# Optimization experiments

Measured on AMD Instinct MI355X. Metric: run time of the kernel, lower is better.

The kernel has to match this reference:

```python
import jax, jax.numpy as jnp
import numpy as np

N = 50000   # num_nodes
D = 128     # h_dim
R = 32      # num_rels * 2 (forward + inverse relations)
B = 8       # num_bases
E = 600000  # num_edges


def setup_inputs() -> dict:
    key = jax.random.key(0)
    ks = jax.random.split(key, 14)
    s = 1.0 / np.sqrt(D)
    return {
        "h_ids": jnp.arange(N, dtype=jnp.int32),
        "src": jax.random.randint(ks[0], (E,), 0, N),
        "dst": jax.random.randint(ks[1], (E,), 0, N),
        "etype": jax.random.randint(ks[2], (E,), 0, R),
        "norm": jax.random.uniform(ks[3], (E, 1), dtype=jnp.float32),
        "embedding": jax.random.normal(ks[4], (N, D), dtype=jnp.float32) * 0.05,
        "w_comp1": jax.random.normal(ks[5], (R, B), dtype=jnp.float32) * (1.0 / np.sqrt(B)),
        "bases1": jax.random.normal(ks[6], (B, D, D), dtype=jnp.float32) * s,
        "loop_w1": jax.random.normal(ks[7], (D, D), dtype=jnp.float32) * s,
        "bias1": jnp.zeros((D,), dtype=jnp.float32),
        "w_comp2": jax.random.normal(ks[8], (R, B), dtype=jnp.float32) * (1.0 / np.sqrt(B)),
        "bases2": jax.random.normal(ks[9], (B, D, D), dtype=jnp.float32) * s,
        "loop_w2": jax.random.normal(ks[10], (D, D), dtype=jnp.float32) * s,
        "bias2": jnp.zeros((D,), dtype=jnp.float32),
    }


def _rel_graph_conv(h, src, dst, etype, norm, w_comp, bases, loop_w, bias, act):
    # basis decomposition: W[r] = sum_b w_comp[r,b] * bases[b]
    W = jnp.einsum('rb,bio->rio', w_comp, bases)          # [R, D, D]
    # transform every node by every relation weight (dense GEMM)
    all_t = jnp.einsum('ni,rio->nro', h, W)               # [N, R, D]
    # per-edge gather of relation-specific transformed source features
    msg = all_t[src, etype] * norm                        # [E, D]
    # scatter-aggregate messages at destination nodes
    agg = jax.ops.segment_sum(msg, dst, num_segments=h.shape[0])  # [N, D]
    out = agg + h @ loop_w + bias                         # self-loop + bias
    return act(out) if act is not None else out


def reference(h_ids, src, dst, etype, norm, embedding,
              w_comp1, bases1, loop_w1, bias1,
              w_comp2, bases2, loop_w2, bias2):
    # EmbeddingLayer
    h = embedding[h_ids]                                  # [N, D]
    # hidden layer 0: relu activation (idx < num_hidden_layers-1)
    h = _rel_graph_conv(h, src, dst, etype, norm, w_comp1, bases1, loop_w1, bias1, jax.nn.relu)
    # hidden layer 1: no activation (last layer)
    h = _rel_graph_conv(h, src, dst, etype, norm, w_comp2, bases2, loop_w2, bias2, None)
    return h
```

## Files before the change

### kernel.cpp

```cpp
#include <hip/hip_runtime.h>

#define DD 128
#define NB 8
#define KTOT 1152

typedef unsigned int uint_t;
typedef __attribute__((ext_vector_type(8))) _Float16 half8v;
typedef __attribute__((ext_vector_type(2))) _Float16 half2v;
typedef __attribute__((ext_vector_type(4))) float f32x4;

static __device__ __forceinline__ void gld_lds16(const _Float16* g, _Float16* l)
{
  __builtin_amdgcn_global_load_lds(
      (const __attribute__((address_space(1))) void*)g,
      (__attribute__((address_space(3))) void*)l, 16, 0, 0);
}

static __device__ __forceinline__ half2v bc_h2(uint_t u)
{
  union { uint_t u; half2v h; } c; c.u = u; return c.h;
}

static __device__ __forceinline__ float fdot2(uint_t a, uint_t b, float acc)
{
#if __has_builtin(__builtin_amdgcn_fdot2)
  return __builtin_amdgcn_fdot2(bc_h2(a), bc_h2(b), acc, false);
#else
  half2v x = bc_h2(a), y = bc_h2(b);
  return acc + (float)x[0] * (float)y[0] + (float)x[1] * (float)y[1];
#endif
}

__global__ __launch_bounds__(256) void k_prep_w(
    const float* __restrict__ bases1, const float* __restrict__ loopw1,
    const float* __restrict__ bases2, const float* __restrict__ loopw2,
    _Float16* __restrict__ WcA)
{
  int i = blockIdx.x * 256 + threadIdx.x;
  if (i >= 2 * 36 * DD * 32) return;
  int layer = i / (36 * DD * 32);
  int rem   = i % (36 * DD * 32);
  int ks    = rem / (DD * 32);
  int rem2  = rem % (DD * 32);
  int feat  = rem2 / 32;
  int j     = rem2 % 32;
  int k     = ks * 32 + j;
  const float* basesL = layer ? bases2 : bases1;
  const float* loopwL = layer ? loopw2 : loopw1;
  float v;
  if (k < 1024) {
    int kk = k >> 3, b = k & 7;
    v = basesL[((size_t)b * DD + kk) * DD + feat];
  } else {
    v = loopwL[(size_t)(k - 1024) * DD + feat];
  }
  WcA[i] = (_Float16)v;
}

__global__ __launch_bounds__(256) void k_cast(
    const float* __restrict__ h, const int* __restrict__ ids,
    _Float16* __restrict__ hf, int N)
{
  int i = blockIdx.x * 256 + threadIdx.x;
  if (i >= N * (DD / 8)) return;
  int n  = i / (DD / 8);
  int k8 = (i % (DD / 8)) * 8;
  int row = ids ? ids[n] : n;
  const float* hp = h + (size_t)row * DD + k8;
  float4 v0 = *(const float4*)hp;
  float4 v1 = *(const float4*)(hp + 4);
  union { _Float16 e[8]; uint4 q; } p;
  p.e[0]=(_Float16)v0.x; p.e[1]=(_Float16)v0.y; p.e[2]=(_Float16)v0.z; p.e[3]=(_Float16)v0.w;
  p.e[4]=(_Float16)v1.x; p.e[5]=(_Float16)v1.y; p.e[6]=(_Float16)v1.z; p.e[7]=(_Float16)v1.w;
  *(uint4*)&hf[(size_t)n * DD + k8] = p.q;
}

__global__ __launch_bounds__(256) void k_zero(int* __restrict__ p, int n)
{
  int i = blockIdx.x * 256 + threadIdx.x;
  if (i < n) p[i] = 0;
}

__global__ __launch_bounds__(256) void k_hist(
    const int* __restrict__ dst, int* __restrict__ cnt, int E)
{
  int e = blockIdx.x * 256 + threadIdx.x;
  if (e < E) atomicAdd(&cnt[dst[e]], 1);
}

__global__ __launch_bounds__(256) void k_bsum(
    const int* __restrict__ cnt, int* __restrict__ bsum, int N)
{
  __shared__ int s[256];
  int i = blockIdx.x * 256 + threadIdx.x;
  s[threadIdx.x] = (i < N) ? ((cnt[i] + 1) & ~1) : 0;
  __syncthreads();
  for (int off = 128; off > 0; off >>= 1) {
    if (threadIdx.x < off) s[threadIdx.x] += s[threadIdx.x + off];
    __syncthreads();
  }
  if (threadIdx.x == 0) bsum[blockIdx.x] = s[0];
}

__global__ __launch_bounds__(256) void k_scanb(
    const int* __restrict__ bsum, int* __restrict__ boff, int nb)
{
  __shared__ int s[256];
  int t = threadIdx.x;
  int own = (t < nb) ? bsum[t] : 0;
  s[t] = own;
  __syncthreads();
  for (int off = 1; off < 256; off <<= 1) {
    int v = (t >= off) ? s[t - off] : 0;
    __syncthreads();
    s[t] += v;
    __syncthreads();
  }
  if (t < nb) boff[t] = s[t] - own;
}

__global__ __launch_bounds__(256) void k_scan3(
    const int* __restrict__ cnt, const int* __restrict__ boff,
    int* __restrict__ row_start, int N)
{
  __shared__ int s[256];
  int t = threadIdx.x;
  int i = blockIdx.x * 256 + t;
  int v = (i < N) ? ((cnt[i] + 1) & ~1) : 0;
  s[t] = v;
  __syncthreads();
  for (int off = 1; off < 256; off <<= 1) {
    int u = (t >= off) ? s[t - off] : 0;
    __syncthreads();
    s[t] += u;
    __syncthreads();
  }
  if (i < N) row_start[i] = boff[blockIdx.x] + s[t] - v;
}

__global__ __launch_bounds__(256) void k_pad(
    const int* __restrict__ rowst, const int* __restrict__ cnt,
    int* __restrict__ psrc, int N)
{
  int v = blockIdx.x * 256 + threadIdx.x;
  if (v < N && (cnt[v] & 1)) {
    int slot = rowst[v] + cnt[v];
    psrc[slot] = 0;
  }
}

__global__ __launch_bounds__(256) void k_place(
    const int* __restrict__ dst, const int* __restrict__ src,
    const int* __restrict__ etype, const float* __restrict__ norm,
    const int* __restrict__ row_start, int* __restrict__ cursor,
    int* __restrict__ psrc, int2* __restrict__ en, int E)
{
  int e = blockIdx.x * 256 + threadIdx.x;
  if (e < E) {
    int v = dst[e];
    int slot = row_start[v] + atomicAdd(&cursor[v], 1);
    psrc[slot] = src[e];
    en[slot] = make_int2(etype[e], __float_as_int(norm[e]));
  }
}

__global__ __launch_bounds__(256) void k_payload_pair(
    const int2* __restrict__ en,
    const float* __restrict__ wcomp1, const float* __restrict__ wcomp2,
    _Float16* __restrict__ c1, _Float16* __restrict__ c2, int npair)
{
  int i = blockIdx.x * 256 + threadIdx.x;
  if (i >= npair) return;
  int2 e0 = en[2 * i], e1 = en[2 * i + 1];
  float n0 = __int_as_float(e0.y), n1 = __int_as_float(e1.y);
  const float* w10 = wcomp1 + e0.x * NB;
  const float* w11 = wcomp1 + e1.x * NB;
  const float* w20 = wcomp2 + e0.x * NB;
  const float* w21 = wcomp2 + e1.x * NB;

  union { _Float16 h[16]; uint4 q[2]; } p;
  #pragma unroll
  for (int b = 0; b < NB; b++) {
    p.h[b * 2]     = (_Float16)(w10[b] * n0);
    p.h[b * 2 + 1] = (_Float16)(w11[b] * n1);
  }
  *(uint4*)&c1[(size_t)i * 16]     = p.q[0];
  *(uint4*)&c1[(size_t)i * 16 + 8] = p.q[1];
  #pragma unroll
  for (int b = 0; b < NB; b++) {
    p.h[b * 2]     = (_Float16)(w20[b] * n0);
    p.h[b * 2 + 1] = (_Float16)(w21[b] * n1);
  }
  *(uint4*)&c2[(size_t)i * 16]     = p.q[0];
  *(uint4*)&c2[(size_t)i * 16 + 8] = p.q[1];
}

__global__ __launch_bounds__(256) void k_agg(
    const int* __restrict__ rowst, const int* __restrict__ cnt,
    const int* __restrict__ psrc, const _Float16* __restrict__ cpair,
    const _Float16* __restrict__ hf,
    _Float16* __restrict__ agg, int N)
{
  int v = blockIdx.x * 4 + (threadIdx.x >> 6);
  if (v >= N) return;
  int lane = threadIdx.x & 63;
  const uint_t* hf32 = (const uint_t*)hf;
  const int beg = rowst[v];
  const int npairs = (cnt[v] + 1) >> 1;
  const uint_t* cp = (const uint_t*)cpair + (size_t)(beg >> 1) * 8;
  const int* ps = psrc + beg;

  float ax[NB] = {}, ay[NB] = {};
  int i = 0;
  for (; i + 2 <= npairs; i += 2) {
    int s0 = ps[2*i + 0], s1 = ps[2*i + 1];
    int s2 = ps[2*i + 2], s3 = ps[2*i + 3];
    uint_t u0 = hf32[(size_t)s0 * 64 + lane];
    uint_t u1 = hf32[(size_t)s1 * 64 + lane];
    uint_t u2 = hf32[(size_t)s2 * 64 + lane];
    uint_t u3 = hf32[(size_t)s3 * 64 + lane];
    uint_t lo01 = __builtin_amdgcn_perm(u0, u1, 0x01000504);
    uint_t hi01 = __builtin_amdgcn_perm(u0, u1, 0x03020706);
    uint_t lo23 = __builtin_amdgcn_perm(u2, u3, 0x01000504);
    uint_t hi23 = __builtin_amdgcn_perm(u2, u3, 0x03020706);
    #pragma unroll
    for (int b = 0; b < NB; b++) {
      uint_t ca = cp[(size_t)i * 8 + b];
      uint_t cb = cp[(size_t)(i + 1) * 8 + b];
      ax[b] = fdot2(ca, lo01, ax[b]);
      ay[b] = fdot2(ca, hi01, ay[b]);
      ax[b] = fdot2(cb, lo23, ax[b]);
      ay[b] = fdot2(cb, hi23, ay[b]);
    }
  }
  if (i < npairs) {
    int s0 = ps[2*i + 0], s1 = ps[2*i + 1];
    uint_t u0 = hf32[(size_t)s0 * 64 + lane];
    uint_t u1 = hf32[(size_t)s1 * 64 + lane];
    uint_t lo01 = __builtin_amdgcn_perm(u0, u1, 0x01000504);
    uint_t hi01 = __builtin_amdgcn_perm(u0, u1, 0x03020706);
    #pragma unroll
    for (int b = 0; b < NB; b++) {
      uint_t ca = cp[(size_t)i * 8 + b];
      ax[b] = fdot2(ca, lo01, ax[b]);
      ay[b] = fdot2(ca, hi01, ay[b]);
    }
  }

  union { _Float16 e[8]; uint4 q; } p0, p1;
  #pragma unroll
  for (int b = 0; b < NB; b++) { p0.e[b] = (_Float16)ax[b]; p1.e[b] = (_Float16)ay[b]; }
  uint4* dstp = (uint4*)&agg[(size_t)v * 1024 + lane * 16];
  dstp[0] = p0.q;
  dstp[1] = p1.q;
}

template <int LAYER>
__global__ __launch_bounds__(256) void k_mm(
    const _Float16* __restrict__ agg,
    const _Float16* __restrict__ hf,
    const _Float16* __restrict__ WcA,
    const float* __restrict__ bias,
    float* __restrict__ outf, _Float16* __restrict__ outh, int N)
{
  __shared__ _Float16 sB[2][2048];

  const int n0   = blockIdx.x * 32;
  const int wv   = threadIdx.x >> 6;
  const int lane = threadIdx.x & 63;
  const int l15  = lane & 15, l4 = lane >> 4;

  int nodeS = n0 + (lane & 31); if (nodeS >= N) nodeS = N - 1;
  const int ksl = 2 * wv + (lane >> 5);

  f32x4 acc[2][2];
  #pragma unroll
  for (int a = 0; a < 2; a++)
    #pragma unroll
    for (int b = 0; b < 2; b++) acc[a][b] = (f32x4)0.f;

  const int fbase = wv * 32 + l15;
  const int koff  = l4 * 8;

  auto STAGE = [&](int buf, int t) {
    const _Float16* g;
    if (t < 16) g = &agg[(size_t)nodeS * 1024 + t * 64 + ksl * 8];
    else        g = &hf [(size_t)nodeS * DD   + (t - 16) * 64 + ksl * 8];
    gld_lds16(g, &sB[buf][2 * wv * 256]);
  };

  auto COMPUTE = [&](int buf, int t) {
    #pragma unroll
    for (int sub = 0; sub < 2; sub++) {
      const int ks = 2 * t + sub;
      half8v af0 = *(const half8v*)&WcA[((size_t)ks * DD + fbase     ) * 32 + koff];
      half8v af1 = *(const half8v*)&WcA[((size_t)ks * DD + fbase + 16) * 32 + koff];
      half8v bf0 = *(const half8v*)&sB[buf][(sub * 4 + l4) * 256 + l15 * 8];
      half8v bf1 = *(const half8v*)&sB[buf][(sub * 4 + l4) * 256 + (16 + l15) * 8];
      acc[0][0] = __builtin_amdgcn_mfma_f32_16x16x32_f16(af0, bf0, acc[0][0], 0, 0, 0);
      acc[0][1] = __builtin_amdgcn_mfma_f32_16x16x32_f16(af0, bf1, acc[0][1], 0, 0, 0);
      acc[1][0] = __builtin_amdgcn_mfma_f32_16x16x32_f16(af1, bf0, acc[1][0], 0, 0, 0);
      acc[1][1] = __builtin_amdgcn_mfma_f32_16x16x32_f16(af1, bf1, acc[1][1], 0, 0, 0);
    }
  };

  STAGE(0, 0);
  int cur = 0;
  for (int t = 0; t < 18; t++) {
    if (t < 17) {
      STAGE(cur ^ 1, t + 1);
      asm volatile("s_waitcnt vmcnt(1)" ::: "memory");
    } else {
      asm volatile("s_waitcnt vmcnt(0)" ::: "memory");
    }
    __builtin_amdgcn_s_barrier();
    __builtin_amdgcn_sched_barrier(0);
    COMPUTE(cur, t);
    __builtin_amdgcn_sched_barrier(0);
    asm volatile("s_waitcnt lgkmcnt(0)" ::: "memory");
    __builtin_amdgcn_s_barrier();
    cur ^= 1;
  }

  #pragma unroll
  for (int mf = 0; mf < 2; mf++)
    #pragma unroll
    for (int nf = 0; nf < 2; nf++) {
      int n = n0 + nf * 16 + l15;
      if (n >= N) continue;
      int feat = wv * 32 + mf * 16 + l4 * 4;
      if (LAYER == 1) {
        union { _Float16 e[4]; uint2 q; } p;
        #pragma unroll
        for (int r = 0; r < 4; r++)
          p.e[r] = (_Float16)fmaxf(acc[mf][nf][r] + bias[feat + r], 0.f);
        *(uint2*)&outh[(size_t)n * DD + feat] = p.q;
      } else {
        float4 o;
        o.x = acc[mf][nf][0] + bias[feat + 0];
        o.y = acc[mf][nf][1] + bias[feat + 1];
        o.z = acc[mf][nf][2] + bias[feat + 2];
        o.w = acc[mf][nf][3] + bias[feat + 3];
        *(float4*)&outf[(size_t)n * DD + feat] = o;
      }
    }
}

extern "C" void kernel_launch(void* const* d_in, const int* in_sizes, int n_in,
                              void* d_out, int out_size, void* d_ws, size_t ws_size,
                              hipStream_t stream)
{
  const int*   h_ids     = (const int*)d_in[0];
  const int*   src       = (const int*)d_in[1];
  const int*   dst       = (const int*)d_in[2];
  const int*   etype     = (const int*)d_in[3];
  const float* norm      = (const float*)d_in[4];
  const float* embedding = (const float*)d_in[5];
  const float* w_comp1   = (const float*)d_in[6];
  const float* bases1    = (const float*)d_in[7];
  const float* loop_w1   = (const float*)d_in[8];
  const float* bias1     = (const float*)d_in[9];
  const float* w_comp2   = (const float*)d_in[10];
  const float* bases2    = (const float*)d_in[11];
  const float* loop_w2   = (const float*)d_in[12];
  const float* bias2     = (const float*)d_in[13];

  const int N = in_sizes[0];
  const int E = in_sizes[1];
  const int S = (E + N) & ~1;
  const int NPAIR = S >> 1;
  const int NBLK = (N + 255) / 256;

  char* base = (char*)d_ws;
  size_t off = 0;
  auto alloc = [&](size_t bytes) -> char* {
    char* p = base + off;
    off += (bytes + 255) & ~(size_t)255;
    return p;
  };
  _Float16* agg  = (_Float16*)alloc((size_t)N * 1024 * 2);
  _Float16* hfp  = (_Float16*)alloc((size_t)N * DD * 2);
  _Float16* h1h  = (_Float16*)alloc((size_t)N * DD * 2);
  _Float16* WcA  = (_Float16*)alloc((size_t)2 * 36 * DD * 32 * 2);
  int*      cnt    = (int*)   alloc((size_t)2 * N * 4);
  int*      cursor = cnt + N;
  int*      rowst  = (int*)   alloc((size_t)N * 4);
  int*      bsum   = (int*)   alloc(256 * 4);
  int*      boff   = (int*)   alloc(256 * 4);
  int*      psrc   = (int*)   alloc((size_t)S * 4);
  int2*     en     = (int2*)  alloc((size_t)S * 8);
  _Float16* c1     = (_Float16*)alloc((size_t)S * 8 * 2);
  _Float16* c2     = (_Float16*)alloc((size_t)S * 8 * 2);
  float*    out    = (float*)d_out;

  k_zero <<<(2 * N + 255) / 256, 256, 0, stream>>>(cnt, 2 * N);
  k_zero <<<(2 * S + 255) / 256, 256, 0, stream>>>((int*)en, 2 * S);
  k_hist <<<(E + 255) / 256, 256, 0, stream>>>(dst, cnt, E);
  k_bsum <<<NBLK, 256, 0, stream>>>(cnt, bsum, N);
  k_scanb<<<1, 256, 0, stream>>>(bsum, boff, NBLK);
  k_scan3<<<NBLK, 256, 0, stream>>>(cnt, boff, rowst, N);
  k_pad  <<<NBLK, 256, 0, stream>>>(rowst, cnt, psrc, N);
  k_place<<<(E + 255) / 256, 256, 0, stream>>>(dst, src, etype, norm,
                                               rowst, cursor, psrc, en, E);
  k_payload_pair<<<(NPAIR + 255) / 256, 256, 0, stream>>>(
      en, w_comp1, w_comp2, c1, c2, NPAIR);

  k_prep_w<<<(2 * 36 * DD * 32 + 255) / 256, 256, 0, stream>>>(bases1, loop_w1, bases2, loop_w2, WcA);

  dim3 gmm((N + 31) / 32);
  int gagg = (N + 3) / 4;

  k_cast<<<(N * (DD / 8) + 255) / 256, 256, 0, stream>>>(embedding, h_ids, hfp, N);
  k_agg<<<gagg, 256, 0, stream>>>(rowst, cnt, psrc, c1, hfp, agg, N);
  k_mm<1><<<gmm, 256, 0, stream>>>(agg, hfp, WcA, bias1, nullptr, h1h, N);

  k_agg<<<gagg, 256, 0, stream>>>(rowst, cnt, psrc, c2, h1h, agg, N);
  k_mm<2><<<gmm, 256, 0, stream>>>(agg, h1h, WcA + (size_t)36 * DD * 32, bias2, out, nullptr, N);
}
```

Before: 298.0 us.

## Fuse pad into scan, merge zero launches, unroll aggregation, simplify GEMM pipeline

```diff
diff --git a/kernel.cpp b/kernel.cpp
--- a/kernel.cpp
+++ b/kernel.cpp
@@ -121,12 +121,13 @@
 
 __global__ __launch_bounds__(256) void k_scan3(
     const int* __restrict__ cnt, const int* __restrict__ boff,
-    int* __restrict__ row_start, int N)
+    int* __restrict__ row_start, int* __restrict__ psrc, int N)
 {
   __shared__ int s[256];
   int t = threadIdx.x;
   int i = blockIdx.x * 256 + t;
-  int v = (i < N) ? ((cnt[i] + 1) & ~1) : 0;
+  int c = (i < N) ? cnt[i] : 0;
+  int v = (c + 1) & ~1;
   s[t] = v;
   __syncthreads();
   for (int off = 1; off < 256; off <<= 1) {
@@ -135,17 +136,10 @@
     s[t] += u;
     __syncthreads();
   }
-  if (i < N) row_start[i] = boff[blockIdx.x] + s[t] - v;
-}
-
-__global__ __launch_bounds__(256) void k_pad(
-    const int* __restrict__ rowst, const int* __restrict__ cnt,
-    int* __restrict__ psrc, int N)
-{
-  int v = blockIdx.x * 256 + threadIdx.x;
-  if (v < N && (cnt[v] & 1)) {
-    int slot = rowst[v] + cnt[v];
-    psrc[slot] = 0;
+  if (i < N) {
+    int rs = boff[blockIdx.x] + s[t] - v;
+    row_start[i] = rs;
+    if (c & 1) psrc[rs + c] = 0;
   }
 }
 
@@ -212,6 +206,26 @@
 
   float ax[NB] = {}, ay[NB] = {};
   int i = 0;
+  for (; i + 4 <= npairs; i += 4) {
+    uint_t u[8], lo[4], hi[4];
+    #pragma unroll
+    for (int q = 0; q < 8; q++)
+      u[q] = hf32[(size_t)ps[2*i + q] * 64 + lane];
+    #pragma unroll
+    for (int q = 0; q < 4; q++) {
+      lo[q] = __builtin_amdgcn_perm(u[2*q], u[2*q+1], 0x01000504);
+      hi[q] = __builtin_amdgcn_perm(u[2*q], u[2*q+1], 0x03020706);
+    }
+    #pragma unroll
+    for (int b = 0; b < NB; b++) {
+      #pragma unroll
+      for (int q = 0; q < 4; q++) {
+        uint_t cc = cp[(size_t)(i + q) * 8 + b];
+        ax[b] = fdot2(cc, lo[q], ax[b]);
+        ay[b] = fdot2(cc, hi[q], ay[b]);
+      }
+    }
+  }
   for (; i + 2 <= npairs; i += 2) {
     int s0 = ps[2*i + 0], s1 = ps[2*i + 1];
     int s2 = ps[2*i + 2], s3 = ps[2*i + 3];
@@ -305,22 +319,15 @@
   };
 
   STAGE(0, 0);
+  __syncthreads();
   int cur = 0;
-  for (int t = 0; t < 18; t++) {
-    if (t < 17) {
-      STAGE(cur ^ 1, t + 1);
-      asm volatile("s_waitcnt vmcnt(1)" ::: "memory");
-    } else {
-      asm volatile("s_waitcnt vmcnt(0)" ::: "memory");
-    }
-    __builtin_amdgcn_s_barrier();
-    __builtin_amdgcn_sched_barrier(0);
+  for (int t = 0; t < 17; t++) {
+    STAGE(cur ^ 1, t + 1);
     COMPUTE(cur, t);
-    __builtin_amdgcn_sched_barrier(0);
-    asm volatile("s_waitcnt lgkmcnt(0)" ::: "memory");
-    __builtin_amdgcn_s_barrier();
+    __syncthreads();
     cur ^= 1;
   }
+  COMPUTE(cur, 17);
 
   #pragma unroll
   for (int mf = 0; mf < 2; mf++)
@@ -384,22 +391,21 @@
   _Float16* WcA  = (_Float16*)alloc((size_t)2 * 36 * DD * 32 * 2);
   int*      cnt    = (int*)   alloc((size_t)2 * N * 4);
   int*      cursor = cnt + N;
+  int2*     en     = (int2*)  alloc((size_t)S * 8);
   int*      rowst  = (int*)   alloc((size_t)N * 4);
   int*      bsum   = (int*)   alloc(256 * 4);
   int*      boff   = (int*)   alloc(256 * 4);
   int*      psrc   = (int*)   alloc((size_t)S * 4);
-  int2*     en     = (int2*)  alloc((size_t)S * 8);
   _Float16* c1     = (_Float16*)alloc((size_t)S * 8 * 2);
   _Float16* c2     = (_Float16*)alloc((size_t)S * 8 * 2);
   float*    out    = (float*)d_out;
 
-  k_zero <<<(2 * N + 255) / 256, 256, 0, stream>>>(cnt, 2 * N);
-  k_zero <<<(2 * S + 255) / 256, 256, 0, stream>>>((int*)en, 2 * S);
+  int zn = (int)(((char*)(en + S) - (char*)cnt) / 4);
+  k_zero <<<(zn + 255) / 256, 256, 0, stream>>>(cnt, zn);
   k_hist <<<(E + 255) / 256, 256, 0, stream>>>(dst, cnt, E);
   k_bsum <<<NBLK, 256, 0, stream>>>(cnt, bsum, N);
   k_scanb<<<1, 256, 0, stream>>>(bsum, boff, NBLK);
-  k_scan3<<<NBLK, 256, 0, stream>>>(cnt, boff, rowst, N);
-  k_pad  <<<NBLK, 256, 0, stream>>>(rowst, cnt, psrc, N);
+  k_scan3<<<NBLK, 256, 0, stream>>>(cnt, boff, rowst, psrc, N);
   k_place<<<(E + 255) / 256, 256, 0, stream>>>(dst, src, etype, norm,
                                                rowst, cursor, psrc, en, E);
   k_payload_pair<<<(NPAIR + 255) / 256, 256, 0, stream>>>(
```

Result: faster. 289.4 us (-2.9%).
